# Kernel tuning notes

Measured on AMD Instinct MI355X. Metric: run time of the kernel, lower is better.

Reference implementation:

```python
import jax, jax.numpy as jnp
import numpy as np

EPS = 1e-5
NEG_INF = float('-inf')

B, L, D = 4, 1024, 1024
H = 16
HD = D // H
I = 3280  # _round_to_multiple(3.2 * 1024, 8)
WIN = 256
STD = 0.01


def rmsnorm(x, w):
    x = jnp.clip(x.astype(jnp.float32), -10000.0, 10000.0)
    rms = jnp.sqrt(jnp.maximum(jnp.mean(x * x, axis=-1, keepdims=True), EPS) + EPS)
    out = x / rms * w
    return jnp.where(jnp.isfinite(out), out, jnp.zeros_like(out))


def setup_inputs() -> dict:
    key = jax.random.key(0)
    ks = jax.random.split(key, 12)
    inp = {
        'x': jax.random.normal(ks[0], (B, L, D), dtype=jnp.float32),
        'wq_w': jax.random.normal(ks[1], (D, D), dtype=jnp.float32) * STD,
        'wq_b': jnp.zeros((D,), jnp.float32),
        'wk_w': jax.random.normal(ks[2], (D, D), dtype=jnp.float32) * STD,
        'wk_b': jnp.zeros((D,), jnp.float32),
        'wv_w': jax.random.normal(ks[3], (D, D), dtype=jnp.float32) * STD,
        'wv_b': jnp.zeros((D,), jnp.float32),
        'wo_w': jax.random.normal(ks[4], (D, D), dtype=jnp.float32) * STD,
        'wo_b': jnp.zeros((D,), jnp.float32),
        'q_norm_w': jnp.ones((HD,), jnp.float32),
        'k_norm_w': jnp.ones((HD,), jnp.float32),
        'seq_norm_w': jnp.ones((D,), jnp.float32),
        'seq_post_norm_w': jnp.ones((D,), jnp.float32),
        'ffn_norm_w': jnp.ones((D,), jnp.float32),
        'ffn_post_norm_w': jnp.ones((D,), jnp.float32),
        'w1_w': jax.random.normal(ks[5], (I, D), dtype=jnp.float32) * STD,
        'w1_b': jnp.zeros((I,), jnp.float32),
        'w2_w': jax.random.normal(ks[6], (D, I), dtype=jnp.float32) * STD,
        'w2_b': jnp.zeros((D,), jnp.float32),
        'w3_w': jax.random.normal(ks[7], (I, D), dtype=jnp.float32) * STD,
        'w3_b': jnp.zeros((I,), jnp.float32),
        'window_size': WIN,
    }
    return inp


def attention(x, wq_w, wq_b, wk_w, wk_b, wv_w, wv_b, wo_w, wo_b, q_norm_w, k_norm_w, window_size):
    b, l, d = x.shape
    x = x.astype(jnp.float32)
    q = (x @ wq_w.T + wq_b).reshape(b, l, H, HD)
    k = (x @ wk_w.T + wk_b).reshape(b, l, H, HD)
    v = (x @ wv_w.T + wv_b).reshape(b, l, H, HD)
    q = rmsnorm(q, q_norm_w)
    k = rmsnorm(k, k_norm_w)
    scale = HD ** -0.5
    scores = jnp.einsum('blhd,bmhd->bhlm', q, k) * scale
    i = jnp.arange(l)[:, None]
    j = jnp.arange(l)[None, :]
    masked = (j > i) | (i - j >= window_size)  # True => forbidden
    scores = scores + jnp.where(masked, NEG_INF, 0.0)
    p = jax.nn.softmax(scores, axis=-1)
    attn = jnp.einsum('bhlm,bmhd->blhd', p, v)
    attn = jnp.where(jnp.isfinite(attn), attn, jnp.zeros_like(attn))
    attn = attn.reshape(b, l, d)
    return attn @ wo_w.T + wo_b


def swiglu(x, w1_w, w1_b, w2_w, w2_b, w3_w, w3_b):
    x = x.astype(jnp.float32)
    z1 = x @ w1_w.T + w1_b
    z3 = x @ w3_w.T + w3_b
    return (jax.nn.silu(z1) * z3) @ w2_w.T + w2_b


def reference(x, wq_w, wq_b, wk_w, wk_b, wv_w, wv_b, wo_w, wo_b,
              q_norm_w, k_norm_w, seq_norm_w, seq_post_norm_w,
              ffn_norm_w, ffn_post_norm_w,
              w1_w, w1_b, w2_w, w2_b, w3_w, w3_b, window_size):
    # seq_norm -> attn -> seq_post_norm -> residual
    a = attention(rmsnorm(x, seq_norm_w), wq_w, wq_b, wk_w, wk_b, wv_w, wv_b,
                  wo_w, wo_b, q_norm_w, k_norm_w, window_size)
    h = x + rmsnorm(a, seq_post_norm_w)
    # ffn_norm -> ffn -> ffn_post_norm -> residual
    f = swiglu(rmsnorm(h, ffn_norm_w), w1_w, w1_b, w2_w, w2_b, w3_w, w3_b)
    return h + rmsnorm(f, ffn_post_norm_w)
```

## Files before the change

kernel.cpp:

```cpp
#include <hip/hip_runtime.h>
#include <cmath>
#include <cstdint>

typedef __bf16 bf16;
typedef bf16 bf16x4 __attribute__((ext_vector_type(4)));
typedef bf16 bf16x8 __attribute__((ext_vector_type(8)));
typedef float f32x4 __attribute__((ext_vector_type(4)));
typedef unsigned int u32;
typedef u32 u32x4 __attribute__((ext_vector_type(4)));

#define EPS 1e-5f

__device__ __forceinline__ float clipf(float v) {
    return fminf(fmaxf(v, -10000.0f), 10000.0f);
}
__device__ __forceinline__ float fin0(float v) { return isfinite(v) ? v : 0.0f; }

__device__ __forceinline__ void async_copy16(void* lds, const void* g) {
    __builtin_amdgcn_global_load_lds((__attribute__((address_space(1))) void*)(void*)g,
                                     (__attribute__((address_space(3))) void*)lds,
                                     16, 0, 0);
}

__global__ __launch_bounds__(256) void convert4(const float* __restrict__ i0, const float* __restrict__ i1,
                                                const float* __restrict__ i2, const float* __restrict__ i3,
                                                bf16* __restrict__ o0, bf16* __restrict__ o1,
                                                bf16* __restrict__ o2, bf16* __restrict__ o3) {
    int z = blockIdx.z;
    const float* in = (z == 0) ? i0 : (z == 1) ? i1 : (z == 2) ? i2 : i3;
    bf16* out = (z == 0) ? o0 : (z == 1) ? o1 : (z == 2) ? o2 : o3;
    int r = blockIdx.x;
    f32x4 v = ((const f32x4*)(in + (size_t)r * 1024))[threadIdx.x];
    bf16x4 o = {(bf16)v[0], (bf16)v[1], (bf16)v[2], (bf16)v[3]};
    ((bf16x4*)(out + (size_t)r * 1024))[threadIdx.x] = o;
}

__global__ __launch_bounds__(256) void convert_w13(const float* __restrict__ i0, const float* __restrict__ i1,
                                                   bf16* __restrict__ o0, bf16* __restrict__ o1) {
    const float* in = blockIdx.z ? i1 : i0;
    bf16* out = blockIdx.z ? o1 : o0;
    int r = blockIdx.x;
    bf16x4 o = {(bf16)0.f, (bf16)0.f, (bf16)0.f, (bf16)0.f};
    if (r < 3280) {
        f32x4 v = ((const f32x4*)(in + (size_t)r * 1024))[threadIdx.x];
        o[0] = (bf16)v[0]; o[1] = (bf16)v[1]; o[2] = (bf16)v[2]; o[3] = (bf16)v[3];
    }
    ((bf16x4*)(out + (size_t)r * 1024))[threadIdx.x] = o;
}

__global__ __launch_bounds__(256) void convert_w2(const float* __restrict__ in, bf16* __restrict__ out) {
    int r = blockIdx.x;
    int c4 = (blockIdx.y * 256 + threadIdx.x) * 4;
    if (c4 >= 3328) return;
    bf16x4 o = {(bf16)0.f, (bf16)0.f, (bf16)0.f, (bf16)0.f};
    if (c4 + 3 < 3280) {
        f32x4 v = *(const f32x4*)(in + (size_t)r * 3280 + c4);
        o[0] = (bf16)v[0]; o[1] = (bf16)v[1]; o[2] = (bf16)v[2]; o[3] = (bf16)v[3];
    } else {
        #pragma unroll
        for (int j = 0; j < 4; ++j)
            if (c4 + j < 3280) o[j] = (bf16)in[(size_t)r * 3280 + c4 + j];
    }
    *(bf16x4*)(out + (size_t)r * 3328 + c4) = o;
}

__device__ __forceinline__ float blockReduceSum(float v, float* sbuf) {
    #pragma unroll
    for (int off = 32; off >= 1; off >>= 1) v += __shfl_xor(v, off, 64);
    int w = threadIdx.x >> 6;
    __syncthreads();
    if ((threadIdx.x & 63) == 0) sbuf[w] = v;
    __syncthreads();
    return sbuf[0] + sbuf[1] + sbuf[2] + sbuf[3];
}

__global__ __launch_bounds__(256) void rmsnorm_in(const float* __restrict__ x,
                                                  const float* __restrict__ w,
                                                  bf16* __restrict__ out) {
    __shared__ float sred[4];
    int row = blockIdx.x, t = threadIdx.x;
    f32x4 xv = ((const f32x4*)(x + (size_t)row * 1024))[t];
    f32x4 cv;
    cv[0] = clipf(xv[0]); cv[1] = clipf(xv[1]); cv[2] = clipf(xv[2]); cv[3] = clipf(xv[3]);
    float ss = cv[0]*cv[0] + cv[1]*cv[1] + cv[2]*cv[2] + cv[3]*cv[3];
    float tot = blockReduceSum(ss, sred);
    float rms = sqrtf(fmaxf(tot * (1.0f / 1024.0f), EPS) + EPS);
    f32x4 wv = ((const f32x4*)w)[t];
    bf16x4 o;
    o[0] = (bf16)fin0(cv[0] / rms * wv[0]);
    o[1] = (bf16)fin0(cv[1] / rms * wv[1]);
    o[2] = (bf16)fin0(cv[2] / rms * wv[2]);
    o[3] = (bf16)fin0(cv[3] / rms * wv[3]);
    *(bf16x4*)(out + (size_t)row * 1024 + t * 4) = o;
}

template <bool EMIT>
__global__ __launch_bounds__(256) void resid_norm(const float* __restrict__ xres,
                                                  const float* __restrict__ p0,
                                                  const float* __restrict__ p1,
                                                  const float* __restrict__ bias,
                                                  const float* __restrict__ wpost,
                                                  const float* __restrict__ wnext,
                                                  float* __restrict__ hout,
                                                  bf16* __restrict__ hnout) {
    __shared__ float sred[4];
    int row = blockIdx.x, t = threadIdx.x;
    f32x4 a0 = ((const f32x4*)(p0 + (size_t)row * 1024))[t];
    f32x4 a1 = ((const f32x4*)(p1 + (size_t)row * 1024))[t];
    f32x4 bv = ((const f32x4*)bias)[t];
    f32x4 af;
    af[0] = clipf(a0[0] + a1[0] + bv[0]);
    af[1] = clipf(a0[1] + a1[1] + bv[1]);
    af[2] = clipf(a0[2] + a1[2] + bv[2]);
    af[3] = clipf(a0[3] + a1[3] + bv[3]);
    float ss = af[0]*af[0] + af[1]*af[1] + af[2]*af[2] + af[3]*af[3];
    float tot = blockReduceSum(ss, sred);
    float rms1 = sqrtf(fmaxf(tot * (1.0f / 1024.0f), EPS) + EPS);
    f32x4 xv = ((const f32x4*)(xres + (size_t)row * 1024))[t];
    f32x4 wp = ((const f32x4*)wpost)[t];
    f32x4 hv;
    hv[0] = xv[0] + fin0(af[0] / rms1 * wp[0]);
    hv[1] = xv[1] + fin0(af[1] / rms1 * wp[1]);
    hv[2] = xv[2] + fin0(af[2] / rms1 * wp[2]);
    hv[3] = xv[3] + fin0(af[3] / rms1 * wp[3]);
    ((f32x4*)(hout + (size_t)row * 1024))[t] = hv;
    if (EMIT) {
        f32x4 cv;
        cv[0] = clipf(hv[0]); cv[1] = clipf(hv[1]); cv[2] = clipf(hv[2]); cv[3] = clipf(hv[3]);
        float ss2 = cv[0]*cv[0] + cv[1]*cv[1] + cv[2]*cv[2] + cv[3]*cv[3];
        float tot2 = blockReduceSum(ss2, sred);
        float rms2 = sqrtf(fmaxf(tot2 * (1.0f / 1024.0f), EPS) + EPS);
        f32x4 wn = ((const f32x4*)wnext)[t];
        bf16x4 o;
        o[0] = (bf16)fin0(cv[0] / rms2 * wn[0]);
        o[1] = (bf16)fin0(cv[1] / rms2 * wn[1]);
        o[2] = (bf16)fin0(cv[2] / rms2 * wn[2]);
        o[3] = (bf16)fin0(cv[3] / rms2 * wn[3]);
        *(bf16x4*)(hnout + (size_t)row * 1024 + t * 4) = o;
    }
}

__global__ __launch_bounds__(256) void gemm_qkv(const bf16* __restrict__ A,
                                                const bf16* __restrict__ B0,
                                                const bf16* __restrict__ B1,
                                                const bf16* __restrict__ B2,
                                                const float* __restrict__ g0,
                                                const float* __restrict__ g1,
                                                const float* __restrict__ g2,
                                                const float* __restrict__ qnw,
                                                const float* __restrict__ knw,
                                                bf16* __restrict__ C0,
                                                bf16* __restrict__ C1,
                                                bf16* __restrict__ VT) {
    const int z = blockIdx.z;
    const bf16* B = (z == 0) ? B0 : (z == 1) ? B1 : B2;
    const float* bias = (z == 0) ? g0 : (z == 1) ? g1 : g2;
    const float* hw = (z == 0) ? qnw : knw;

    __shared__ __align__(16) bf16 sA[2][128 * 32];
    __shared__ __align__(16) bf16 sB[2][128 * 32];
    const int tid = threadIdx.x;
    const int w = tid >> 6, lane = tid & 63;
    const int m0 = blockIdx.x * 128;
    const int n0 = blockIdx.y * 128;
    const int mwo = (w >> 1) * 64, nwo = (w & 1) * 64;
    const int r16 = lane & 15, quad = lane >> 4;
    const int kreg = quad * 8;
    const int K = 1024, N = 1024;

    f32x4 zero = {0.f, 0.f, 0.f, 0.f};
    f32x4 acc[4][4];
    #pragma unroll
    for (int i = 0; i < 4; ++i)
        #pragma unroll
        for (int j = 0; j < 4; ++j) acc[i][j] = zero;

    const int c0 = tid, c1 = tid + 256;
    const int am0 = c0 >> 2, ak0 = (c0 & 3) << 3;
    const int am1 = c1 >> 2, ak1 = (c1 & 3) << 3;

    {
        async_copy16(&sA[0][c0 * 8], &A[(size_t)(m0 + am0) * K + ak0]);
        async_copy16(&sA[0][c1 * 8], &A[(size_t)(m0 + am1) * K + ak1]);
        async_copy16(&sB[0][c0 * 8], &B[(size_t)(n0 + am0) * K + ak0]);
        async_copy16(&sB[0][c1 * 8], &B[(size_t)(n0 + am1) * K + ak1]);
    }
    for (int kt = 0; kt < 32; ++kt) {
        __syncthreads();
        const int cur = kt & 1, nxt = cur ^ 1;
        if (kt + 1 < 32) {
            const int kb = (kt + 1) << 5;
// ... 16 lines not shown
    }

    float bv[4];
    #pragma unroll
    for (int ni = 0; ni < 4; ++ni) bv[ni] = bias[n0 + nwo + ni * 16 + r16];

    if (z < 2) {
        bf16* C = (z == 0) ? C0 : C1;
        float nwv[4];
        #pragma unroll
        for (int ni = 0; ni < 4; ++ni) nwv[ni] = hw[ni * 16 + r16];
        #pragma unroll
        for (int mi = 0; mi < 4; ++mi) {
            #pragma unroll
            for (int r = 0; r < 4; ++r) {
                float v[4], ss = 0.0f;
                #pragma unroll
                for (int ni = 0; ni < 4; ++ni) {
                    v[ni] = clipf(acc[mi][ni][r] + bv[ni]);
                    ss += v[ni] * v[ni];
                }
                ss += __shfl_xor(ss, 1, 64);
                ss += __shfl_xor(ss, 2, 64);
                ss += __shfl_xor(ss, 4, 64);
                ss += __shfl_xor(ss, 8, 64);
                float rms = sqrtf(fmaxf(ss * (1.0f / 64.0f), EPS) + EPS);
                int row = m0 + mwo + mi * 16 + quad * 4 + r;
                #pragma unroll
                for (int ni = 0; ni < 4; ++ni) {
                    int col = n0 + nwo + ni * 16 + r16;
                    C[(size_t)row * N + col] = (bf16)fin0(v[ni] / rms * nwv[ni]);
                }
            }
        }
    } else {
        const int b_ = m0 >> 10;
        const int tokbase = (m0 & 1023) + mwo;
        #pragma unroll
        for (int ni = 0; ni < 4; ++ni) {
            int col = n0 + nwo + ni * 16 + r16;
            int h_ = col >> 6, hd = col & 63;
            bf16* dst = VT + (((size_t)b_ * 16 + h_) * 64 + hd) * 1024;
            #pragma unroll
            for (int mi = 0; mi < 4; ++mi) {
                bf16x4 pack;
                #pragma unroll
                for (int r = 0; r < 4; ++r) pack[r] = (bf16)(acc[mi][ni][r] + bv[ni]);
                *(bf16x4*)&dst[tokbase + mi * 16 + quad * 4] = pack;
            }
        }
    }
}

__global__ __launch_bounds__(512) void gemm_ffn1(const bf16* __restrict__ A,
                                                 const bf16* __restrict__ B1,
                                                 const bf16* __restrict__ B3,
                                                 const float* __restrict__ b1,
                                                 const float* __restrict__ b3,
                                                 bf16* __restrict__ G) {
    __shared__ __align__(16) bf16 sA[2][128 * 32];
    __shared__ __align__(16) bf16 sB1[2][128 * 32];
    __shared__ __align__(16) bf16 sB3[2][128 * 32];
    const int tid = threadIdx.x;
    const int w = tid >> 6, lane = tid & 63;
    const int m0 = blockIdx.x * 128;
    const int n0 = blockIdx.y * 128;
    const int mwo = (w >> 2) * 64, nwo = (w & 3) * 32;
    const int r16 = lane & 15, quad = lane >> 4;
    const int kreg = quad * 8;
    const int K = 1024, N = 3328;

    f32x4 zero = {0.f, 0.f, 0.f, 0.f};
    f32x4 acc1[4][2], acc3[4][2];
    #pragma unroll
    for (int i = 0; i < 4; ++i)
        #pragma unroll
        for (int j = 0; j < 2; ++j) { acc1[i][j] = zero; acc3[i][j] = zero; }

    const int arow = tid >> 2, akoff = (tid & 3) << 3;

    {
        async_copy16(&sA[0][tid * 8],  &A[(size_t)(m0 + arow) * K + akoff]);
        async_copy16(&sB1[0][tid * 8], &B1[(size_t)(n0 + arow) * K + akoff]);
        async_copy16(&sB3[0][tid * 8], &B3[(size_t)(n0 + arow) * K + akoff]);
    }
    for (int kt = 0; kt < 32; ++kt) {
        __syncthreads();
        const int cur = kt & 1, nxt = cur ^ 1;
        if (kt + 1 < 32) {
            const int kb = (kt + 1) << 5;
            async_copy16(&sA[nxt][tid * 8],  &A[(size_t)(m0 + arow) * K + kb + akoff]);
            async_copy16(&sB1[nxt][tid * 8], &B1[(size_t)(n0 + arow) * K + kb + akoff]);
            async_copy16(&sB3[nxt][tid * 8], &B3[(size_t)(n0 + arow) * K + kb + akoff]);
        }
        bf16x8 af[4], bf1[2], bf3[2];
        #pragma unroll
        for (int i = 0; i < 4; ++i)
            af[i]  = *(const bf16x8*)&sA[cur][(mwo + i * 16 + r16) * 32 + kreg];
        #pragma unroll
        for (int i = 0; i < 2; ++i) {
            bf1[i] = *(const bf16x8*)&sB1[cur][(nwo + i * 16 + r16) * 32 + kreg];
            bf3[i] = *(const bf16x8*)&sB3[cur][(nwo + i * 16 + r16) * 32 + kreg];
        }
        #pragma unroll
        for (int mi = 0; mi < 4; ++mi)
            #pragma unroll
            for (int ni = 0; ni < 2; ++ni) {
                acc1[mi][ni] = __builtin_amdgcn_mfma_f32_16x16x32_bf16(af[mi], bf1[ni], acc1[mi][ni], 0, 0, 0);
                acc3[mi][ni] = __builtin_amdgcn_mfma_f32_16x16x32_bf16(af[mi], bf3[ni], acc3[mi][ni], 0, 0, 0);
            }
    }

    #pragma unroll
    for (int ni = 0; ni < 2; ++ni) {
        int col = n0 + nwo + ni * 16 + r16;
        float bv1 = (col < 3280) ? b1[col] : 0.0f;
        float bv3 = (col < 3280) ? b3[col] : 0.0f;
        #pragma unroll
        for (int mi = 0; mi < 4; ++mi) {
            #pragma unroll
            for (int r = 0; r < 4; ++r) {
                int row = m0 + mwo + mi * 16 + quad * 4 + r;
                float z1 = acc1[mi][ni][r] + bv1;
                float z3 = acc3[mi][ni][r] + bv3;
                float s = z1 / (1.0f + __expf(-z1));
                G[(size_t)row * N + col] = (bf16)(s * z3);
            }
        }
    }
}

__global__ __launch_bounds__(256) void gemm_splitk(const bf16* __restrict__ A,
                                                   const bf16* __restrict__ B,
                                                   float* __restrict__ P,
                                                   int N, int K, int Kh) {
    const int s = blockIdx.z;
    __shared__ __align__(16) bf16 sA[2][128 * 32];
    __shared__ __align__(16) bf16 sB[2][128 * 32];
    const int tid = threadIdx.x;
    const int w = tid >> 6, lane = tid & 63;
    const int m0 = blockIdx.x * 128;
    const int n0 = blockIdx.y * 128;
    const int mwo = (w >> 1) * 64, nwo = (w & 1) * 64;
    const int r16 = lane & 15, quad = lane >> 4;
    const int kreg = quad * 8;
    const int kbase = s * Kh;

    f32x4 zero = {0.f, 0.f, 0.f, 0.f};
    f32x4 acc[4][4];
    #pragma unroll
    for (int i = 0; i < 4; ++i)
        #pragma unroll
        for (int j = 0; j < 4; ++j) acc[i][j] = zero;

    const int c0 = tid, c1 = tid + 256;
    const int am0 = c0 >> 2, ak0 = (c0 & 3) << 3;
    const int am1 = c1 >> 2, ak1 = (c1 & 3) << 3;
    const int kIters = Kh >> 5;

    {
        async_copy16(&sA[0][c0 * 8], &A[(size_t)(m0 + am0) * K + kbase + ak0]);
        async_copy16(&sA[0][c1 * 8], &A[(size_t)(m0 + am1) * K + kbase + ak1]);
        async_copy16(&sB[0][c0 * 8], &B[(size_t)(n0 + am0) * K + kbase + ak0]);
        async_copy16(&sB[0][c1 * 8], &B[(size_t)(n0 + am1) * K + kbase + ak1]);
    }
    for (int kt = 0; kt < kIters; ++kt) {
        __syncthreads();
        const int cur = kt & 1, nxt = cur ^ 1;
        if (kt + 1 < kIters) {
            const int kb = kbase + ((kt + 1) << 5);
            async_copy16(&sA[nxt][c0 * 8], &A[(size_t)(m0 + am0) * K + kb + ak0]);
            async_copy16(&sA[nxt][c1 * 8], &A[(size_t)(m0 + am1) * K + kb + ak1]);
            async_copy16(&sB[nxt][c0 * 8], &B[(size_t)(n0 + am0) * K + kb + ak0]);
            async_copy16(&sB[nxt][c1 * 8], &B[(size_t)(n0 + am1) * K + kb + ak1]);
        }
        bf16x8 af[4], bfr[4];
        #pragma unroll
        for (int i = 0; i < 4; ++i) {
            af[i]  = *(const bf16x8*)&sA[cur][(mwo + i * 16 + r16) * 32 + kreg];
            bfr[i] = *(const bf16x8*)&sB[cur][(nwo + i * 16 + r16) * 32 + kreg];
        }
        #pragma unroll
        for (int mi = 0; mi < 4; ++mi)
            #pragma unroll
            for (int ni = 0; ni < 4; ++ni)
                acc[mi][ni] = __builtin_amdgcn_mfma_f32_16x16x32_bf16(af[mi], bfr[ni], acc[mi][ni], 0, 0, 0);
    }

    float* Pz = P + (size_t)s * 4096 * 1024;
    #pragma unroll
    for (int mi = 0; mi < 4; ++mi)
        #pragma unroll
        for (int ni = 0; ni < 4; ++ni) {
            int col = n0 + nwo + ni * 16 + r16;
            #pragma unroll
            for (int r = 0; r < 4; ++r) {
                int row = m0 + mwo + mi * 16 + quad * 4 + r;
                Pz[(size_t)row * N + col] = acc[mi][ni][r];
            }
        }
}

__global__ __launch_bounds__(256) void attn_win(const bf16* __restrict__ q,
                                                const bf16* __restrict__ k,
                                                const bf16* __restrict__ vt,
                                                const int* __restrict__ winp,
                                                bf16* __restrict__ o) {
    __shared__ __align__(16) bf16 sQ[64 * 64];
    __shared__ __align__(16) bf16 sK[64 * 64];
    __shared__ __align__(16) bf16 sVt[64 * 80];
    __shared__ __align__(16) bf16 sP[64 * 64];
    const int tid = threadIdx.x, w = tid >> 6, lane = tid & 63;
    const int qt = blockIdx.x, h = blockIdx.y, b = blockIdx.z;
    const int q0 = qt * 64;
    const int win = *winp;
    const float scale = 0.125f;
    const int r16 = lane & 15, quad = lane >> 4;

    {
        int qr0 = tid >> 3, col0 = (tid & 7) * 8;
        async_copy16(&sQ[tid * 8], &q[(((size_t)b * 1024 + q0 + qr0) * 16 + h) * 64 + col0]);
        int c1 = tid + 256;
        int qr1 = c1 >> 3, col1 = (c1 & 7) * 8;
        async_copy16(&sQ[c1 * 8], &q[(((size_t)b * 1024 + q0 + qr1) * 16 + h) * 64 + col1]);
    }
    __syncthreads();
    bf16x8 aq0 = *(const bf16x8*)&sQ[(w * 16 + r16) * 64 + quad * 8];
    bf16x8 aq1 = *(const bf16x8*)&sQ[(w * 16 + r16) * 64 + 32 + quad * 8];

    float M[4], Lr[4];
    f32x4 zero = {0.f, 0.f, 0.f, 0.f};
    f32x4 accO[4];
    #pragma unroll
    for (int r = 0; r < 4; ++r) { M[r] = -INFINITY; Lr[r] = 0.0f; }
    #pragma unroll
    for (int nf = 0; nf < 4; ++nf) accO[nf] = zero;

    int lo = q0 - (win - 1); if (lo < 0) lo = 0;
    const int kt0 = lo >> 6;
    const bf16* vth = vt + ((size_t)b * 16 + h) * 64 * 1024;

    for (int kt = kt0; kt <= qt; ++kt) {
        __syncthreads();
        {
            int kr0 = tid >> 3, col0 = (tid & 7) * 8;
            async_copy16(&sK[tid * 8], &k[(((size_t)b * 1024 + kt * 64 + kr0) * 16 + h) * 64 + col0]);
            int c1 = tid + 256;
            int kr1 = c1 >> 3, col1 = (c1 & 7) * 8;
            async_copy16(&sK[c1 * 8], &k[(((size_t)b * 1024 + kt * 64 + kr1) * 16 + h) * 64 + col1]);
        }
        #pragma unroll
        for (int c = tid; c < 512; c += 256) {
            int hd = c >> 3, koff = (c & 7) * 8;
            *(u32x4*)&sVt[hd * 80 + koff] = *(const u32x4*)&vth[(size_t)hd * 1024 + kt * 64 + koff];
        }
// ... 15 lines not shown
            int i = q0 + w * 16 + quad * 4 + r;
            float p[4];
            float rowmax = -INFINITY;
            #pragma unroll
            for (int nf = 0; nf < 4; ++nf) {
                int j = kt * 64 + nf * 16 + r16;
                bool ok = (j <= i) && (i - j < win);
                float sv = ok ? sf[nf][r] * scale : -INFINITY;
                p[nf] = sv;
                rowmax = fmaxf(rowmax, sv);
            }
            #pragma unroll
            for (int off = 1; off < 16; off <<= 1)
                rowmax = fmaxf(rowmax, __shfl_xor(rowmax, off, 64));
            float mnew = fmaxf(M[r], rowmax);
            float alpha = (mnew == M[r]) ? 1.0f : __expf(M[r] - mnew);
            float rs = 0.0f;
            #pragma unroll
            for (int nf = 0; nf < 4; ++nf) {
                float pv = (p[nf] == -INFINITY) ? 0.0f : __expf(p[nf] - mnew);
                rs += pv;
                sP[(w * 16 + quad * 4 + r) * 64 + nf * 16 + r16] = (bf16)pv;
            }
            #pragma unroll
            for (int off = 1; off < 16; off <<= 1) rs += __shfl_xor(rs, off, 64);
            Lr[r] = Lr[r] * alpha + rs;
            M[r] = mnew;
            #pragma unroll
            for (int nf = 0; nf < 4; ++nf) accO[nf][r] = accO[nf][r] * alpha;
        }
        __syncthreads();

        bf16x8 ap0 = *(const bf16x8*)&sP[(w * 16 + r16) * 64 + quad * 8];
        bf16x8 ap1 = *(const bf16x8*)&sP[(w * 16 + r16) * 64 + 32 + quad * 8];
        #pragma unroll
        for (int nf = 0; nf < 4; ++nf) {
            bf16x8 bv0 = *(const bf16x8*)&sVt[(nf * 16 + r16) * 80 + quad * 8];
            bf16x8 bv1 = *(const bf16x8*)&sVt[(nf * 16 + r16) * 80 + 32 + quad * 8];
            accO[nf] = __builtin_amdgcn_mfma_f32_16x16x32_bf16(ap0, bv0, accO[nf], 0, 0, 0);
            accO[nf] = __builtin_amdgcn_mfma_f32_16x16x32_bf16(ap1, bv1, accO[nf], 0, 0, 0);
        }
    }

    #pragma unroll
    for (int r = 0; r < 4; ++r) {
        float inv = (Lr[r] > 0.0f) ? 1.0f / Lr[r] : 0.0f;
        int row = q0 + w * 16 + quad * 4 + r;
        #pragma unroll
        for (int nf = 0; nf < 4; ++nf) {
            float ov = fin0(accO[nf][r] * inv);
            o[(((size_t)b * 1024 + row) * 16 + h) * 64 + nf * 16 + r16] = (bf16)ov;
        }
    }
}

extern "C" void kernel_launch(void* const* d_in, const int* in_sizes, int n_in,
                              void* d_out, int out_size, void* d_ws, size_t ws_size,
                              hipStream_t stream) {
    const float* x       = (const float*)d_in[0];
    const float* wq_w    = (const float*)d_in[1];
    const float* wq_b    = (const float*)d_in[2];
    const float* wk_w    = (const float*)d_in[3];
    const float* wk_b    = (const float*)d_in[4];
    const float* wv_w    = (const float*)d_in[5];
    const float* wv_b    = (const float*)d_in[6];
    const float* wo_w    = (const float*)d_in[7];
    const float* wo_b    = (const float*)d_in[8];
    const float* q_norm_w= (const float*)d_in[9];
    const float* k_norm_w= (const float*)d_in[10];
    const float* seq_norm_w      = (const float*)d_in[11];
    const float* seq_post_norm_w = (const float*)d_in[12];
    const float* ffn_norm_w      = (const float*)d_in[13];
    const float* ffn_post_norm_w = (const float*)d_in[14];
    const float* w1_w    = (const float*)d_in[15];
    const float* w1_b    = (const float*)d_in[16];
    const float* w2_w    = (const float*)d_in[17];
    const float* w2_b    = (const float*)d_in[18];
    const float* w3_w    = (const float*)d_in[19];
    const float* w3_b    = (const float*)d_in[20];
    const int*   winp    = (const int*)d_in[21];
    float* out = (float*)d_out;

    const size_t SZ_W   = 2097152;
    const size_t SZ_WP  = 6815744;
    const size_t SZ_ACT = 8388608;
    const size_t SZ_H   = 16777216;
    const size_t SZ_P   = 33554432;

    char* p = (char*)d_ws;
    bf16* Wq  = (bf16*)p; p += SZ_W;
    bf16* Wk  = (bf16*)p; p += SZ_W;
    bf16* Wv  = (bf16*)p; p += SZ_W;
    bf16* Wo  = (bf16*)p; p += SZ_W;
    bf16* W1p = (bf16*)p; p += SZ_WP;
    bf16* W3p = (bf16*)p; p += SZ_WP;
    bf16* W2p = (bf16*)p; p += SZ_WP;
    float* h  = (float*)p; p += SZ_H;
    bf16* hn  = (bf16*)p; p += SZ_ACT;
    float* part = (float*)p; p += SZ_P;
    char* regionA = p;
    bf16* xn    = (bf16*)(regionA);
    bf16* qb    = (bf16*)(regionA + 1 * SZ_ACT);
    bf16* kb    = (bf16*)(regionA + 2 * SZ_ACT);
    bf16* vtb   = (bf16*)(regionA + 3 * SZ_ACT);
    bf16* attnb = (bf16*)(regionA + 4 * SZ_ACT);
    bf16* g     = (bf16*)(regionA);

    dim3 blk(256);

    convert4<<<dim3(1024, 1, 4), blk, 0, stream>>>(wq_w, wk_w, wv_w, wo_w, Wq, Wk, Wv, Wo);
    convert_w13<<<dim3(3328, 1, 2), blk, 0, stream>>>(w1_w, w3_w, W1p, W3p);
    convert_w2<<<dim3(1024, 4, 1), blk, 0, stream>>>(w2_w, W2p);

    rmsnorm_in<<<4096, blk, 0, stream>>>(x, seq_norm_w, xn);

    gemm_qkv<<<dim3(32, 8, 3), blk, 0, stream>>>(xn, Wq, Wk, Wv, wq_b, wk_b, wv_b,
                                                 q_norm_w, k_norm_w, qb, kb, vtb);

    attn_win<<<dim3(16, 16, 4), blk, 0, stream>>>(qb, kb, vtb, winp, attnb);

    gemm_splitk<<<dim3(32, 8, 2), blk, 0, stream>>>(attnb, Wo, part, 1024, 1024, 512);

    resid_norm<true><<<4096, blk, 0, stream>>>(x, part, part + 4096 * 1024, wo_b,
                                               seq_post_norm_w, ffn_norm_w, h, hn);

    gemm_ffn1<<<dim3(32, 26), dim3(512), 0, stream>>>(hn, W1p, W3p, w1_b, w3_b, g);

    gemm_splitk<<<dim3(32, 8, 2), blk, 0, stream>>>(g, W2p, part, 1024, 3328, 1664);

    resid_norm<false><<<4096, blk, 0, stream>>>(h, part, part + 4096 * 1024, w2_b,
                                                ffn_post_norm_w, nullptr, out, nullptr);
}
```

Baseline: 382.0 us.

## Merge weight prep into one kernel and fuse tail into cooperative persistent kernel

Merges the three weight-conversion kernels and the input RMSNorm into a single prep launch. The output-projection GEMM, residual norm, FFN1, FFN2 and final residual norm now run as phases of one cooperative kernel, separated by grid-wide syncs, with a fallback to separate launches. This removes launch overhead and gaps between kernels. In exchange the FFN1 phase loses its double-buffered async copies and now syncs twice per k-step, and the 512-block grid limits parallelism per phase.

```diff
diff --git a/kernel.cpp b/kernel.cpp
--- a/kernel.cpp
+++ b/kernel.cpp
@@ -1,6 +1,9 @@
 #include <hip/hip_runtime.h>
+#include <hip/hip_cooperative_groups.h>
 #include <cmath>
 #include <cstdint>
+
+namespace cg = cooperative_groups;
 
 typedef __bf16 bf16;
 typedef bf16 bf16x4 __attribute__((ext_vector_type(4)));
@@ -22,121 +25,69 @@
                                      16, 0, 0);
 }
 
-__global__ __launch_bounds__(256) void convert4(const float* __restrict__ i0, const float* __restrict__ i1,
-                                                const float* __restrict__ i2, const float* __restrict__ i3,
-                                                bf16* __restrict__ o0, bf16* __restrict__ o1,
-                                                bf16* __restrict__ o2, bf16* __restrict__ o3) {
-    int z = blockIdx.z;
-    const float* in = (z == 0) ? i0 : (z == 1) ? i1 : (z == 2) ? i2 : i3;
-    bf16* out = (z == 0) ? o0 : (z == 1) ? o1 : (z == 2) ? o2 : o3;
-    int r = blockIdx.x;
-    f32x4 v = ((const f32x4*)(in + (size_t)r * 1024))[threadIdx.x];
-    bf16x4 o = {(bf16)v[0], (bf16)v[1], (bf16)v[2], (bf16)v[3]};
-    ((bf16x4*)(out + (size_t)r * 1024))[threadIdx.x] = o;
-}
-
-__global__ __launch_bounds__(256) void convert_w13(const float* __restrict__ i0, const float* __restrict__ i1,
-                                                   bf16* __restrict__ o0, bf16* __restrict__ o1) {
-    const float* in = blockIdx.z ? i1 : i0;
-    bf16* out = blockIdx.z ? o1 : o0;
-    int r = blockIdx.x;
-    bf16x4 o = {(bf16)0.f, (bf16)0.f, (bf16)0.f, (bf16)0.f};
-    if (r < 3280) {
-        f32x4 v = ((const f32x4*)(in + (size_t)r * 1024))[threadIdx.x];
-        o[0] = (bf16)v[0]; o[1] = (bf16)v[1]; o[2] = (bf16)v[2]; o[3] = (bf16)v[3];
-    }
-    ((bf16x4*)(out + (size_t)r * 1024))[threadIdx.x] = o;
-}
-
-__global__ __launch_bounds__(256) void convert_w2(const float* __restrict__ in, bf16* __restrict__ out) {
-    int r = blockIdx.x;
-    int c4 = (blockIdx.y * 256 + threadIdx.x) * 4;
-    if (c4 >= 3328) return;
-    bf16x4 o = {(bf16)0.f, (bf16)0.f, (bf16)0.f, (bf16)0.f};
-    if (c4 + 3 < 3280) {
-        f32x4 v = *(const f32x4*)(in + (size_t)r * 3280 + c4);
-        o[0] = (bf16)v[0]; o[1] = (bf16)v[1]; o[2] = (bf16)v[2]; o[3] = (bf16)v[3];
+__global__ __launch_bounds__(256) void prep(const float* __restrict__ wq, const float* __restrict__ wk,
+                                            const float* __restrict__ wv, const float* __restrict__ wo,
+                                            bf16* __restrict__ Wq, bf16* __restrict__ Wk,
+                                            bf16* __restrict__ Wv, bf16* __restrict__ Wo,
+                                            const float* __restrict__ w1, const float* __restrict__ w3,
+                                            bf16* __restrict__ W1p, bf16* __restrict__ W3p,
+                                            const float* __restrict__ w2, bf16* __restrict__ W2p,
+                                            const float* __restrict__ x, const float* __restrict__ snw,
+                                            bf16* __restrict__ xn) {
+    const int bid = blockIdx.x, t = threadIdx.x;
+    if (bid < 4096) {
+        int z = bid >> 10, r = bid & 1023;
+        const float* in = (z == 0) ? wq : (z == 1) ? wk : (z == 2) ? wv : wo;
+        bf16* out = (z == 0) ? Wq : (z == 1) ? Wk : (z == 2) ? Wv : Wo;
+        f32x4 v = ((const f32x4*)(in + (size_t)r * 1024))[t];
+        bf16x4 o = {(bf16)v[0], (bf16)v[1], (bf16)v[2], (bf16)v[3]};
+        ((bf16x4*)(out + (size_t)r * 1024))[t] = o;
+    } else if (bid < 10752) {
+        int b2 = bid - 4096;
+        int which = b2 >= 3328;
+        int r = b2 - (which ? 3328 : 0);
+        const float* in = which ? w3 : w1;
+        bf16* out = which ? W3p : W1p;
+        bf16x4 o = {(bf16)0.f, (bf16)0.f, (bf16)0.f, (bf16)0.f};
+        if (r < 3280) {
+            f32x4 v = ((const f32x4*)(in + (size_t)r * 1024))[t];
+            o[0] = (bf16)v[0]; o[1] = (bf16)v[1]; o[2] = (bf16)v[2]; o[3] = (bf16)v[3];
+        }
+        ((bf16x4*)(out + (size_t)r * 1024))[t] = o;
+    } else if (bid < 11776) {
+        int r = bid - 10752;
+        for (int c4 = t * 4; c4 < 3328; c4 += 1024) {
+            bf16x4 o = {(bf16)0.f, (bf16)0.f, (bf16)0.f, (bf16)0.f};
+            if (c4 + 3 < 3280) {
+                f32x4 v = *(const f32x4*)(w2 + (size_t)r * 3280 + c4);
+                o[0] = (bf16)v[0]; o[1] = (bf16)v[1]; o[2] = (bf16)v[2]; o[3] = (bf16)v[3];
+            } else {
+                #pragma unroll
+                for (int j = 0; j < 4; ++j)
+                    if (c4 + j < 3280) o[j] = (bf16)w2[(size_t)r * 3280 + c4 + j];
+            }
+            *(bf16x4*)(W2p + (size_t)r * 3328 + c4) = o;
+        }
     } else {
-        #pragma unroll
-        for (int j = 0; j < 4; ++j)
-            if (c4 + j < 3280) o[j] = (bf16)in[(size_t)r * 3280 + c4 + j];
-    }
-    *(bf16x4*)(out + (size_t)r * 3328 + c4) = o;
-}
-
-__device__ __forceinline__ float blockReduceSum(float v, float* sbuf) {
-    #pragma unroll
-    for (int off = 32; off >= 1; off >>= 1) v += __shfl_xor(v, off, 64);
-    int w = threadIdx.x >> 6;
-    __syncthreads();
-    if ((threadIdx.x & 63) == 0) sbuf[w] = v;
-    __syncthreads();
-    return sbuf[0] + sbuf[1] + sbuf[2] + sbuf[3];
-}
-
-__global__ __launch_bounds__(256) void rmsnorm_in(const float* __restrict__ x,
-                                                  const float* __restrict__ w,
-                                                  bf16* __restrict__ out) {
-    __shared__ float sred[4];
-    int row = blockIdx.x, t = threadIdx.x;
-    f32x4 xv = ((const f32x4*)(x + (size_t)row * 1024))[t];
-    f32x4 cv;
-    cv[0] = clipf(xv[0]); cv[1] = clipf(xv[1]); cv[2] = clipf(xv[2]); cv[3] = clipf(xv[3]);
-    float ss = cv[0]*cv[0] + cv[1]*cv[1] + cv[2]*cv[2] + cv[3]*cv[3];
-    float tot = blockReduceSum(ss, sred);
-    float rms = sqrtf(fmaxf(tot * (1.0f / 1024.0f), EPS) + EPS);
-    f32x4 wv = ((const f32x4*)w)[t];
-    bf16x4 o;
-    o[0] = (bf16)fin0(cv[0] / rms * wv[0]);
-    o[1] = (bf16)fin0(cv[1] / rms * wv[1]);
-    o[2] = (bf16)fin0(cv[2] / rms * wv[2]);
-    o[3] = (bf16)fin0(cv[3] / rms * wv[3]);
-    *(bf16x4*)(out + (size_t)row * 1024 + t * 4) = o;
-}
-
-template <bool EMIT>
-__global__ __launch_bounds__(256) void resid_norm(const float* __restrict__ xres,
-                                                  const float* __restrict__ p0,
-                                                  const float* __restrict__ p1,
-                                                  const float* __restrict__ bias,
-                                                  const float* __restrict__ wpost,
-                                                  const float* __restrict__ wnext,
-                                                  float* __restrict__ hout,
-                                                  bf16* __restrict__ hnout) {
-    __shared__ float sred[4];
-    int row = blockIdx.x, t = threadIdx.x;
-    f32x4 a0 = ((const f32x4*)(p0 + (size_t)row * 1024))[t];
-    f32x4 a1 = ((const f32x4*)(p1 + (size_t)row * 1024))[t];
-    f32x4 bv = ((const f32x4*)bias)[t];
-    f32x4 af;
-    af[0] = clipf(a0[0] + a1[0] + bv[0]);
-    af[1] = clipf(a0[1] + a1[1] + bv[1]);
-    af[2] = clipf(a0[2] + a1[2] + bv[2]);
-    af[3] = clipf(a0[3] + a1[3] + bv[3]);
-    float ss = af[0]*af[0] + af[1]*af[1] + af[2]*af[2] + af[3]*af[3];
-    float tot = blockReduceSum(ss, sred);
-    float rms1 = sqrtf(fmaxf(tot * (1.0f / 1024.0f), EPS) + EPS);
-    f32x4 xv = ((const f32x4*)(xres + (size_t)row * 1024))[t];
-    f32x4 wp = ((const f32x4*)wpost)[t];
-    f32x4 hv;
-    hv[0] = xv[0] + fin0(af[0] / rms1 * wp[0]);
-    hv[1] = xv[1] + fin0(af[1] / rms1 * wp[1]);
-    hv[2] = xv[2] + fin0(af[2] / rms1 * wp[2]);
-    hv[3] = xv[3] + fin0(af[3] / rms1 * wp[3]);
-    ((f32x4*)(hout + (size_t)row * 1024))[t] = hv;
-    if (EMIT) {
+        __shared__ float sred[4];
+        int row = bid - 11776;
+        f32x4 xv = ((const f32x4*)(x + (size_t)row * 1024))[t];
         f32x4 cv;
-        cv[0] = clipf(hv[0]); cv[1] = clipf(hv[1]); cv[2] = clipf(hv[2]); cv[3] = clipf(hv[3]);
-        float ss2 = cv[0]*cv[0] + cv[1]*cv[1] + cv[2]*cv[2] + cv[3]*cv[3];
-        float tot2 = blockReduceSum(ss2, sred);
-        float rms2 = sqrtf(fmaxf(tot2 * (1.0f / 1024.0f), EPS) + EPS);
-        f32x4 wn = ((const f32x4*)wnext)[t];
+        cv[0] = clipf(xv[0]); cv[1] = clipf(xv[1]); cv[2] = clipf(xv[2]); cv[3] = clipf(xv[3]);
+        float ss = cv[0]*cv[0] + cv[1]*cv[1] + cv[2]*cv[2] + cv[3]*cv[3];
+        #pragma unroll
+        for (int off = 32; off >= 1; off >>= 1) ss += __shfl_xor(ss, off, 64);
+        if ((t & 63) == 0) sred[t >> 6] = ss;
+        __syncthreads();
+        float tot = sred[0] + sred[1] + sred[2] + sred[3];
+        float rms = sqrtf(fmaxf(tot * (1.0f / 1024.0f), EPS) + EPS);
+        f32x4 wv_ = ((const f32x4*)snw)[t];
         bf16x4 o;
-        o[0] = (bf16)fin0(cv[0] / rms2 * wn[0]);
-        o[1] = (bf16)fin0(cv[1] / rms2 * wn[1]);
-        o[2] = (bf16)fin0(cv[2] / rms2 * wn[2]);
-        o[3] = (bf16)fin0(cv[3] / rms2 * wn[3]);
-        *(bf16x4*)(hnout + (size_t)row * 1024 + t * 4) = o;
+        o[0] = (bf16)fin0(cv[0] / rms * wv_[0]);
+        o[1] = (bf16)fin0(cv[1] / rms * wv_[1]);
+        o[2] = (bf16)fin0(cv[2] / rms * wv_[2]);
+        o[3] = (bf16)fin0(cv[3] / rms * wv_[3]);
+        *(bf16x4*)(xn + (size_t)row * 1024 + t * 4) = o;
     }
 }
 
@@ -259,155 +210,6 @@
     }
 }
 
-__global__ __launch_bounds__(512) void gemm_ffn1(const bf16* __restrict__ A,
-                                                 const bf16* __restrict__ B1,
-                                                 const bf16* __restrict__ B3,
-                                                 const float* __restrict__ b1,
-                                                 const float* __restrict__ b3,
-                                                 bf16* __restrict__ G) {
-    __shared__ __align__(16) bf16 sA[2][128 * 32];
-    __shared__ __align__(16) bf16 sB1[2][128 * 32];
-    __shared__ __align__(16) bf16 sB3[2][128 * 32];
-    const int tid = threadIdx.x;
-    const int w = tid >> 6, lane = tid & 63;
-    const int m0 = blockIdx.x * 128;
-    const int n0 = blockIdx.y * 128;
-    const int mwo = (w >> 2) * 64, nwo = (w & 3) * 32;
-    const int r16 = lane & 15, quad = lane >> 4;
-    const int kreg = quad * 8;
-    const int K = 1024, N = 3328;
-
-    f32x4 zero = {0.f, 0.f, 0.f, 0.f};
-    f32x4 acc1[4][2], acc3[4][2];
-    #pragma unroll
-    for (int i = 0; i < 4; ++i)
-        #pragma unroll
-        for (int j = 0; j < 2; ++j) { acc1[i][j] = zero; acc3[i][j] = zero; }
-
-    const int arow = tid >> 2, akoff = (tid & 3) << 3;
-
-    {
-        async_copy16(&sA[0][tid * 8],  &A[(size_t)(m0 + arow) * K + akoff]);
-        async_copy16(&sB1[0][tid * 8], &B1[(size_t)(n0 + arow) * K + akoff]);
-        async_copy16(&sB3[0][tid * 8], &B3[(size_t)(n0 + arow) * K + akoff]);
-    }
-    for (int kt = 0; kt < 32; ++kt) {
-        __syncthreads();
-        const int cur = kt & 1, nxt = cur ^ 1;
-        if (kt + 1 < 32) {
-            const int kb = (kt + 1) << 5;
-            async_copy16(&sA[nxt][tid * 8],  &A[(size_t)(m0 + arow) * K + kb + akoff]);
-            async_copy16(&sB1[nxt][tid * 8], &B1[(size_t)(n0 + arow) * K + kb + akoff]);
-            async_copy16(&sB3[nxt][tid * 8], &B3[(size_t)(n0 + arow) * K + kb + akoff]);
-        }
-        bf16x8 af[4], bf1[2], bf3[2];
-        #pragma unroll
-        for (int i = 0; i < 4; ++i)
-            af[i]  = *(const bf16x8*)&sA[cur][(mwo + i * 16 + r16) * 32 + kreg];
-        #pragma unroll
-        for (int i = 0; i < 2; ++i) {
-            bf1[i] = *(const bf16x8*)&sB1[cur][(nwo + i * 16 + r16) * 32 + kreg];
-            bf3[i] = *(const bf16x8*)&sB3[cur][(nwo + i * 16 + r16) * 32 + kreg];
-        }
-        #pragma unroll
-        for (int mi = 0; mi < 4; ++mi)
-            #pragma unroll
-            for (int ni = 0; ni < 2; ++ni) {
-                acc1[mi][ni] = __builtin_amdgcn_mfma_f32_16x16x32_bf16(af[mi], bf1[ni], acc1[mi][ni], 0, 0, 0);
-                acc3[mi][ni] = __builtin_amdgcn_mfma_f32_16x16x32_bf16(af[mi], bf3[ni], acc3[mi][ni], 0, 0, 0);
-            }
-    }
-
-    #pragma unroll
-    for (int ni = 0; ni < 2; ++ni) {
-        int col = n0 + nwo + ni * 16 + r16;
-        float bv1 = (col < 3280) ? b1[col] : 0.0f;
-        float bv3 = (col < 3280) ? b3[col] : 0.0f;
-        #pragma unroll
-        for (int mi = 0; mi < 4; ++mi) {
-            #pragma unroll
-            for (int r = 0; r < 4; ++r) {
-                int row = m0 + mwo + mi * 16 + quad * 4 + r;
-                float z1 = acc1[mi][ni][r] + bv1;
-                float z3 = acc3[mi][ni][r] + bv3;
-                float s = z1 / (1.0f + __expf(-z1));
-                G[(size_t)row * N + col] = (bf16)(s * z3);
-            }
-        }
-    }
-}
-
-__global__ __launch_bounds__(256) void gemm_splitk(const bf16* __restrict__ A,
-                                                   const bf16* __restrict__ B,
-                                                   float* __restrict__ P,
-                                                   int N, int K, int Kh) {
-    const int s = blockIdx.z;
-    __shared__ __align__(16) bf16 sA[2][128 * 32];
-    __shared__ __align__(16) bf16 sB[2][128 * 32];
-    const int tid = threadIdx.x;
-    const int w = tid >> 6, lane = tid & 63;
-    const int m0 = blockIdx.x * 128;
-    const int n0 = blockIdx.y * 128;
-    const int mwo = (w >> 1) * 64, nwo = (w & 1) * 64;
-    const int r16 = lane & 15, quad = lane >> 4;
-    const int kreg = quad * 8;
-    const int kbase = s * Kh;
-
-    f32x4 zero = {0.f, 0.f, 0.f, 0.f};
-    f32x4 acc[4][4];
-    #pragma unroll
-    for (int i = 0; i < 4; ++i)
-        #pragma unroll
-        for (int j = 0; j < 4; ++j) acc[i][j] = zero;
-
-    const int c0 = tid, c1 = tid + 256;
-    const int am0 = c0 >> 2, ak0 = (c0 & 3) << 3;
-    const int am1 = c1 >> 2, ak1 = (c1 & 3) << 3;
-    const int kIters = Kh >> 5;
-
-    {
-        async_copy16(&sA[0][c0 * 8], &A[(size_t)(m0 + am0) * K + kbase + ak0]);
-        async_copy16(&sA[0][c1 * 8], &A[(size_t)(m0 + am1) * K + kbase + ak1]);
-        async_copy16(&sB[0][c0 * 8], &B[(size_t)(n0 + am0) * K + kbase + ak0]);
-        async_copy16(&sB[0][c1 * 8], &B[(size_t)(n0 + am1) * K + kbase + ak1]);
-    }
-    for (int kt = 0; kt < kIters; ++kt) {
-        __syncthreads();
-        const int cur = kt & 1, nxt = cur ^ 1;
-        if (kt + 1 < kIters) {
-            const int kb = kbase + ((kt + 1) << 5);
-            async_copy16(&sA[nxt][c0 * 8], &A[(size_t)(m0 + am0) * K + kb + ak0]);
-            async_copy16(&sA[nxt][c1 * 8], &A[(size_t)(m0 + am1) * K + kb + ak1]);
-            async_copy16(&sB[nxt][c0 * 8], &B[(size_t)(n0 + am0) * K + kb + ak0]);
-            async_copy16(&sB[nxt][c1 * 8], &B[(size_t)(n0 + am1) * K + kb + ak1]);
-        }
-        bf16x8 af[4], bfr[4];
-        #pragma unroll
-        for (int i = 0; i < 4; ++i) {
-            af[i]  = *(const bf16x8*)&sA[cur][(mwo + i * 16 + r16) * 32 + kreg];
-            bfr[i] = *(const bf16x8*)&sB[cur][(nwo + i * 16 + r16) * 32 + kreg];
-        }
-        #pragma unroll
-        for (int mi = 0; mi < 4; ++mi)
-            #pragma unroll
-            for (int ni = 0; ni < 4; ++ni)
-                acc[mi][ni] = __builtin_amdgcn_mfma_f32_16x16x32_bf16(af[mi], bfr[ni], acc[mi][ni], 0, 0, 0);
-    }
-
-    float* Pz = P + (size_t)s * 4096 * 1024;
-    #pragma unroll
-    for (int mi = 0; mi < 4; ++mi)
-        #pragma unroll
-        for (int ni = 0; ni < 4; ++ni) {
-            int col = n0 + nwo + ni * 16 + r16;
-            #pragma unroll
-            for (int r = 0; r < 4; ++r) {
-                int row = m0 + mwo + mi * 16 + quad * 4 + r;
-                Pz[(size_t)row * N + col] = acc[mi][ni][r];
-            }
-        }
-}
-
 __global__ __launch_bounds__(256) void attn_win(const bf16* __restrict__ q,
                                                 const bf16* __restrict__ k,
                                                 const bf16* __restrict__ vt,
@@ -529,6 +331,245 @@
             o[(((size_t)b * 1024 + row) * 16 + h) * 64 + nf * 16 + r16] = (bf16)ov;
         }
     }
+}
+
+
+__device__ __forceinline__ void phase_splitk(const bf16* __restrict__ A, const bf16* __restrict__ B,
+                                             float* __restrict__ P, int K, int Kh, char* smem) {
+    const int N = 1024;
+    const int tile = blockIdx.x;
+    const int s = tile >> 8;
+    const int mt = tile & 31, nt = (tile >> 5) & 7;
+    const int m0 = mt * 128, n0 = nt * 128;
+    const int kbase = s * Kh;
+    bf16* sA[2] = {(bf16*)smem, (bf16*)(smem + 16384)};
+    bf16* sB[2] = {(bf16*)(smem + 8192), (bf16*)(smem + 24576)};
+
+    const int tid = threadIdx.x;
+    const int w = tid >> 6, lane = tid & 63;
+    const int mwo = (w >> 2) * 64, nwo = (w & 3) * 32;
+    const int r16 = lane & 15, quad = lane >> 4;
+    const int kreg = quad * 8;
+    const int arow = tid >> 2, akoff = (tid & 3) << 3;
+    const int kIters = Kh >> 5;
+
+    f32x4 zero = {0.f, 0.f, 0.f, 0.f};
+    f32x4 acc[4][2];
+    #pragma unroll
+    for (int i = 0; i < 4; ++i)
+        #pragma unroll
+        for (int j = 0; j < 2; ++j) acc[i][j] = zero;
+
+    __syncthreads();
+    async_copy16(&sA[0][tid * 8], &A[(size_t)(m0 + arow) * K + kbase + akoff]);
+    async_copy16(&sB[0][tid * 8], &B[(size_t)(n0 + arow) * K + kbase + akoff]);
+    for (int kt = 0; kt < kIters; ++kt) {
+        __syncthreads();
+        const int cur = kt & 1, nxt = cur ^ 1;
+        if (kt + 1 < kIters) {
+            const int kb = kbase + ((kt + 1) << 5);
+            async_copy16(&sA[nxt][tid * 8], &A[(size_t)(m0 + arow) * K + kb + akoff]);
+            async_copy16(&sB[nxt][tid * 8], &B[(size_t)(n0 + arow) * K + kb + akoff]);
+        }
+        bf16x8 af[4], bfr[2];
+        #pragma unroll
+        for (int i = 0; i < 4; ++i)
+            af[i] = *(const bf16x8*)&sA[cur][(mwo + i * 16 + r16) * 32 + kreg];
+        #pragma unroll
+        for (int i = 0; i < 2; ++i)
+            bfr[i] = *(const bf16x8*)&sB[cur][(nwo + i * 16 + r16) * 32 + kreg];
+        #pragma unroll
+        for (int mi = 0; mi < 4; ++mi)
+            #pragma unroll
+            for (int ni = 0; ni < 2; ++ni)
+                acc[mi][ni] = __builtin_amdgcn_mfma_f32_16x16x32_bf16(af[mi], bfr[ni], acc[mi][ni], 0, 0, 0);
+    }
+    float* Pz = P + (size_t)s * 4096 * 1024;
+    #pragma unroll
+    for (int mi = 0; mi < 4; ++mi)
+        #pragma unroll
+        for (int ni = 0; ni < 2; ++ni) {
+            int col = n0 + nwo + ni * 16 + r16;
+            #pragma unroll
+            for (int r = 0; r < 4; ++r) {
+                int row = m0 + mwo + mi * 16 + quad * 4 + r;
+                Pz[(size_t)row * N + col] = acc[mi][ni][r];
+            }
+        }
+}
+
+__device__ __forceinline__ void phase_resid(const float* __restrict__ xres,
+                                            const float* __restrict__ p0,
+                                            const float* __restrict__ p1,
+                                            const float* __restrict__ bias,
+                                            const float* __restrict__ wpost,
+                                            const float* __restrict__ wnext,
+                                            float* __restrict__ hout,
+                                            bf16* __restrict__ hnout,
+                                            bool emit, float* sred ) {
+    const int tid = threadIdx.x;
+    const int grp = tid >> 8, t = tid & 255;
+    const int w4 = (tid >> 6) & 3;
+    for (int it = 0; it < 4; ++it) {
+        int row = it * 1024 + blockIdx.x * 2 + grp;
+        f32x4 a0 = ((const f32x4*)(p0 + (size_t)row * 1024))[t];
+        f32x4 a1 = ((const f32x4*)(p1 + (size_t)row * 1024))[t];
+        f32x4 bv = ((const f32x4*)bias)[t];
+        f32x4 af;
+        af[0] = clipf(a0[0] + a1[0] + bv[0]);
+        af[1] = clipf(a0[1] + a1[1] + bv[1]);
+        af[2] = clipf(a0[2] + a1[2] + bv[2]);
+        af[3] = clipf(a0[3] + a1[3] + bv[3]);
+        float ss = af[0]*af[0] + af[1]*af[1] + af[2]*af[2] + af[3]*af[3];
+        #pragma unroll
+        for (int off = 32; off >= 1; off >>= 1) ss += __shfl_xor(ss, off, 64);
+        __syncthreads();
+        if ((tid & 63) == 0) sred[grp * 4 + w4] = ss;
+        __syncthreads();
+        float tot = sred[grp*4+0] + sred[grp*4+1] + sred[grp*4+2] + sred[grp*4+3];
+        float rms1 = sqrtf(fmaxf(tot * (1.0f / 1024.0f), EPS) + EPS);
+        f32x4 xv = ((const f32x4*)(xres + (size_t)row * 1024))[t];
+        f32x4 wp = ((const f32x4*)wpost)[t];
+        f32x4 hv;
+        hv[0] = xv[0] + fin0(af[0] / rms1 * wp[0]);
+        hv[1] = xv[1] + fin0(af[1] / rms1 * wp[1]);
+        hv[2] = xv[2] + fin0(af[2] / rms1 * wp[2]);
+        hv[3] = xv[3] + fin0(af[3] / rms1 * wp[3]);
+        ((f32x4*)(hout + (size_t)row * 1024))[t] = hv;
+        if (emit) {
+            f32x4 cv;
+            cv[0] = clipf(hv[0]); cv[1] = clipf(hv[1]); cv[2] = clipf(hv[2]); cv[3] = clipf(hv[3]);
+            float ss2 = cv[0]*cv[0] + cv[1]*cv[1] + cv[2]*cv[2] + cv[3]*cv[3];
+            #pragma unroll
+            for (int off = 32; off >= 1; off >>= 1) ss2 += __shfl_xor(ss2, off, 64);
+            __syncthreads();
+            if ((tid & 63) == 0) sred[grp * 4 + w4] = ss2;
+            __syncthreads();
+            float tot2 = sred[grp*4+0] + sred[grp*4+1] + sred[grp*4+2] + sred[grp*4+3];
+            float rms2 = sqrtf(fmaxf(tot2 * (1.0f / 1024.0f), EPS) + EPS);
+            f32x4 wn = ((const f32x4*)wnext)[t];
+            bf16x4 o;
+            o[0] = (bf16)fin0(cv[0] / rms2 * wn[0]);
+            o[1] = (bf16)fin0(cv[1] / rms2 * wn[1]);
+            o[2] = (bf16)fin0(cv[2] / rms2 * wn[2]);
+            o[3] = (bf16)fin0(cv[3] / rms2 * wn[3]);
+            *(bf16x4*)(hnout + (size_t)row * 1024 + t * 4) = o;
+        }
+    }
+}
+
+__device__ __forceinline__ void phase_ffn1(const bf16* __restrict__ A,
+                                           const bf16* __restrict__ B1,
+                                           const bf16* __restrict__ B3,
+                                           const float* __restrict__ b1,
+                                           const float* __restrict__ b3,
+                                           bf16* __restrict__ G, char* smem) {
+    const int K = 1024, N = 3328;
+    const int tid = threadIdx.x;
+    const int w = tid >> 6, lane = tid & 63;
+    const int mwo = (w >> 2) * 64, nwo = (w & 3) * 32;
+    const int r16 = lane & 15, quad = lane >> 4;
+    const int kreg = quad * 8;
+    const int arow = tid >> 2, akoff = (tid & 3) << 3;
+    bf16* sA  = (bf16*)smem;
+    bf16* sB1 = (bf16*)(smem + 8192);
+    bf16* sB3 = (bf16*)(smem + 16384);
+
+    for (int tile = blockIdx.x; tile < 832; tile += gridDim.x) {
+        const int m0 = (tile & 31) << 7;
+        const int n0 = (tile >> 5) << 7;
+
+        f32x4 zero = {0.f, 0.f, 0.f, 0.f};
+        f32x4 acc1[4][2], acc3[4][2];
+        #pragma unroll
+        for (int i = 0; i < 4; ++i)
+            #pragma unroll
+            for (int j = 0; j < 2; ++j) { acc1[i][j] = zero; acc3[i][j] = zero; }
+
+        for (int kt = 0; kt < 32; ++kt) {
+            const int kb = kt << 5;
+            __syncthreads();
+            async_copy16(&sA[tid * 8],  &A[(size_t)(m0 + arow) * K + kb + akoff]);
+            async_copy16(&sB1[tid * 8], &B1[(size_t)(n0 + arow) * K + kb + akoff]);
+            async_copy16(&sB3[tid * 8], &B3[(size_t)(n0 + arow) * K + kb + akoff]);
+            __syncthreads();
+            bf16x8 af[4], bf1[2], bf3[2];
+            #pragma unroll
+            for (int i = 0; i < 4; ++i)
+                af[i] = *(const bf16x8*)&sA[(mwo + i * 16 + r16) * 32 + kreg];
+            #pragma unroll
+            for (int i = 0; i < 2; ++i) {
+                bf1[i] = *(const bf16x8*)&sB1[(nwo + i * 16 + r16) * 32 + kreg];
+                bf3[i] = *(const bf16x8*)&sB3[(nwo + i * 16 + r16) * 32 + kreg];
+            }
+            #pragma unroll
+            for (int mi = 0; mi < 4; ++mi)
+                #pragma unroll
+                for (int ni = 0; ni < 2; ++ni) {
+                    acc1[mi][ni] = __builtin_amdgcn_mfma_f32_16x16x32_bf16(af[mi], bf1[ni], acc1[mi][ni], 0, 0, 0);
+                    acc3[mi][ni] = __builtin_amdgcn_mfma_f32_16x16x32_bf16(af[mi], bf3[ni], acc3[mi][ni], 0, 0, 0);
+                }
+        }
+        #pragma unroll
+        for (int ni = 0; ni < 2; ++ni) {
+            int col = n0 + nwo + ni * 16 + r16;
+            float bv1 = (col < 3280) ? b1[col] : 0.0f;
+            float bv3 = (col < 3280) ? b3[col] : 0.0f;
+            #pragma unroll
+            for (int mi = 0; mi < 4; ++mi) {
+                #pragma unroll
+                for (int r = 0; r < 4; ++r) {
+                    int row = m0 + mwo + mi * 16 + quad * 4 + r;
+                    float z1 = acc1[mi][ni][r] + bv1;
+                    float z3 = acc3[mi][ni][r] + bv3;
+                    float s = z1 / (1.0f + __expf(-z1));
+                    G[(size_t)row * N + col] = (bf16)(s * z3);
+                }
+            }
+        }
+    }
+}
+
+__global__ __launch_bounds__(512, 4) void coop_tail(const bf16* attnb, const bf16* Wo, float* part,
+                                                    const float* x, const float* wo_b,
+                                                    const float* seq_post_w, const float* ffn_norm_w,
+                                                    float* h, bf16* hn,
+                                                    const bf16* W1p, const bf16* W3p,
+                                                    const float* w1_b, const float* w3_b, bf16* g,
+                                                    const bf16* W2p, const float* w2_b,
+                                                    const float* ffn_post_w, float* out) {
+    __shared__ __align__(16) char smem[32768];
+    cg::grid_group grid = cg::this_grid();
+
+    phase_splitk(attnb, Wo, part, 1024, 512, smem);
+    grid.sync();
+    phase_resid(x, part, part + (size_t)4096 * 1024, wo_b, seq_post_w, ffn_norm_w,
+                h, hn, true, (float*)smem);
+    grid.sync();
+    phase_ffn1(hn, W1p, W3p, w1_b, w3_b, g, smem);
+    grid.sync();
+    phase_splitk(g, W2p, part, 3328, 1664, smem);
+    grid.sync();
+    phase_resid(h, part, part + (size_t)4096 * 1024, w2_b, ffn_post_w, nullptr,
+                out, nullptr, false, (float*)smem);
+}
+
+__global__ __launch_bounds__(512, 4) void tail_splitk(const bf16* __restrict__ A, const bf16* __restrict__ B,
+                                                      float* __restrict__ P, int K, int Kh) {
+    __shared__ __align__(16) char smem[32768];
+    phase_splitk(A, B, P, K, Kh, smem);
+}
+template <bool EMIT>
+__global__ __launch_bounds__(512, 4) void tail_resid(const float* xres, const float* p0, const float* p1,
+                                                     const float* bias, const float* wpost, const float* wnext,
+                                                     float* hout, bf16* hnout) {
+    __shared__ float sred[8];
+    phase_resid(xres, p0, p1, bias, wpost, wnext, hout, hnout, EMIT, sred);
+}
+__global__ __launch_bounds__(512, 4) void tail_ffn1(const bf16* A, const bf16* B1, const bf16* B3,
+                                                    const float* b1, const float* b3, bf16* G) {
+    __shared__ __align__(16) char smem[24576];
+    phase_ffn1(A, B1, B3, b1, b3, G, smem);
 }
 
 extern "C" void kernel_launch(void* const* d_in, const int* in_sizes, int n_in,
@@ -583,28 +624,42 @@
     bf16* attnb = (bf16*)(regionA + 4 * SZ_ACT);
     bf16* g     = (bf16*)(regionA);
 
-    dim3 blk(256);
-
-    convert4<<<dim3(1024, 1, 4), blk, 0, stream>>>(wq_w, wk_w, wv_w, wo_w, Wq, Wk, Wv, Wo);
-    convert_w13<<<dim3(3328, 1, 2), blk, 0, stream>>>(w1_w, w3_w, W1p, W3p);
-    convert_w2<<<dim3(1024, 4, 1), blk, 0, stream>>>(w2_w, W2p);
-
-    rmsnorm_in<<<4096, blk, 0, stream>>>(x, seq_norm_w, xn);
-
-    gemm_qkv<<<dim3(32, 8, 3), blk, 0, stream>>>(xn, Wq, Wk, Wv, wq_b, wk_b, wv_b,
-                                                 q_norm_w, k_norm_w, qb, kb, vtb);
-
-    attn_win<<<dim3(16, 16, 4), blk, 0, stream>>>(qb, kb, vtb, winp, attnb);
-
-    gemm_splitk<<<dim3(32, 8, 2), blk, 0, stream>>>(attnb, Wo, part, 1024, 1024, 512);
-
-    resid_norm<true><<<4096, blk, 0, stream>>>(x, part, part + 4096 * 1024, wo_b,
-                                               seq_post_norm_w, ffn_norm_w, h, hn);
-
-    gemm_ffn1<<<dim3(32, 26), dim3(512), 0, stream>>>(hn, W1p, W3p, w1_b, w3_b, g);
-
-    gemm_splitk<<<dim3(32, 8, 2), blk, 0, stream>>>(g, W2p, part, 1024, 3328, 1664);
-
-    resid_norm<false><<<4096, blk, 0, stream>>>(h, part, part + 4096 * 1024, w2_b,
-                                                ffn_post_norm_w, nullptr, out, nullptr);
-}
+    prep<<<dim3(15872), dim3(256), 0, stream>>>(wq_w, wk_w, wv_w, wo_w, Wq, Wk, Wv, Wo,
+                                                w1_w, w3_w, W1p, W3p, w2_w, W2p,
+                                                x, seq_norm_w, xn);
+
+    gemm_qkv<<<dim3(32, 8, 3), dim3(256), 0, stream>>>(xn, Wq, Wk, Wv, wq_b, wk_b, wv_b,
+                                                       q_norm_w, k_norm_w, qb, kb, vtb);
+
+    attn_win<<<dim3(16, 16, 4), dim3(256), 0, stream>>>(qb, kb, vtb, winp, attnb);
+
+    float* part1 = part + (size_t)4096 * 1024;
+    const float* xc = x;
+    void* args[] = {
+        (void*)&attnb, (void*)&Wo, (void*)&part,
+        (void*)&xc, (void*)&wo_b,
+        (void*)&seq_post_norm_w, (void*)&ffn_norm_w,
+        (void*)&h, (void*)&hn,
+        (void*)&W1p, (void*)&W3p,
+        (void*)&w1_b, (void*)&w3_b, (void*)&g,
+        (void*)&W2p, (void*)&w2_b,
+        (void*)&ffn_post_norm_w, (void*)&out
+    };
+    int maxBlk = 0;
+    hipError_t qerr = hipOccupancyMaxActiveBlocksPerMultiprocessor(&maxBlk, (const void*)coop_tail, 512, 0);
+    bool coop_ok = (qerr == hipSuccess && maxBlk >= 2);
+    if (coop_ok) {
+        hipError_t lerr = hipLaunchCooperativeKernel((void*)coop_tail, dim3(512), dim3(512),
+                                                     args, 0, stream);
+        if (lerr != hipSuccess) { (void)hipGetLastError(); coop_ok = false; }
+    }
+    if (!coop_ok) {
+        tail_splitk<<<dim3(512), dim3(512), 0, stream>>>(attnb, Wo, part, 1024, 512);
+        tail_resid<true><<<dim3(512), dim3(512), 0, stream>>>(x, part, part1, wo_b,
+                                                              seq_post_norm_w, ffn_norm_w, h, hn);
+        tail_ffn1<<<dim3(832), dim3(512), 0, stream>>>(hn, W1p, W3p, w1_b, w3_b, g);
+        tail_splitk<<<dim3(512), dim3(512), 0, stream>>>(g, W2p, part, 3328, 1664);
+        tail_resid<false><<<dim3(512), dim3(512), 0, stream>>>(h, part, part1, w2_b,
+                                                               ffn_post_norm_w, nullptr, out, nullptr);
+    }
+}
```

New measurement: 389.8 us. 2.0% more time.
